# Kernel tuning notes

Measured on AMD Instinct MI355X. Metric: run time of the kernel, lower is better.

The kernel has to match this reference:

```python
import jax, jax.numpy as jnp
import numpy as np

DIM = 768
NUM_HEADS = 12
HEAD_DIM = DIM // NUM_HEADS
SCALE = HEAD_DIM ** (-0.5)
MASK_VAL = -10000000.0


def setup_inputs() -> dict:
    key = jax.random.key(0)
    k1, k2, k3, k4 = jax.random.split(key, 4)
    B, N = 2, 2048
    inputs = jax.random.normal(k1, (B, N, DIM), dtype=jnp.float32)
    padding_mask = jax.random.randint(k2, (B, N), 0, 2, dtype=jnp.int32)
    # Xavier-uniform-ish scaled weights
    w_qkv = jax.random.normal(k3, (3 * DIM, DIM), dtype=jnp.float32) * (1.0 / np.sqrt(DIM))
    w_fc = jax.random.normal(k4, (DIM, DIM), dtype=jnp.float32) * (1.0 / np.sqrt(DIM))
    b_fc = jnp.zeros((DIM,), dtype=jnp.float32)
    return {"inputs": inputs, "padding_mask": padding_mask,
            "w_qkv": w_qkv, "w_fc": w_fc, "b_fc": b_fc}


def reference(inputs, padding_mask, w_qkv, w_fc, b_fc):
    B, N, C = inputs.shape
    # qkv projection (torch Linear: x @ W^T), no bias
    qkv = jnp.einsum('bnc,dc->bnd', inputs, w_qkv)          # [B, N, 3*C]
    qkv = qkv.reshape(B, N, 3, NUM_HEADS, HEAD_DIM)
    qkv = jnp.transpose(qkv, (2, 0, 3, 1, 4))               # [3, B, H, N, hd]
    q, k, v = qkv[0], qkv[1], qkv[2]
    # scores: [B, H, N, N]
    att = jnp.einsum('bhqd,bhkd->bhqk', q, k) * SCALE
    mask = padding_mask[:, None, None, :]                   # [B,1,1,N]
    att = jnp.where(mask > 0, MASK_VAL, att)
    att = jax.nn.softmax(att, axis=-1)
    x = jnp.einsum('bhqk,bhkd->bhqd', att, v)               # [B,H,N,hd]
    x = jnp.transpose(x, (0, 2, 1, 3)).reshape(B, N, C)
    x = jnp.einsum('bnc,dc->bnd', x, w_fc) + b_fc
    return x
```

## Files before the change

### kernel.cpp

```cpp
#include <hip/hip_runtime.h>
#include <hip/hip_bf16.h>

#define DIM_  768
#define NH    12
#define HD    64
#define BB    2
#define NN    2048
#define MM    (BB*NN)
#define QKVD  (3*DIM_)

typedef __attribute__((ext_vector_type(8))) short          bf16x8;
typedef __attribute__((ext_vector_type(4))) float          f32x4;

__device__ __forceinline__ unsigned short f2bf(float f) {
    __hip_bfloat16 h = __float2bfloat16(f);
    unsigned short u; __builtin_memcpy(&u, &h, 2); return u;
}

__device__ __forceinline__ unsigned int cvt_pk_bf16(float lo, float hi) {
    unsigned int r;
    asm("v_cvt_pk_bf16_f32 %0, %1, %2" : "=v"(r) : "v"(lo), "v"(hi));
    return r;
}

__device__ __forceinline__ void gload16(const void* g, void* lds) {
    __builtin_amdgcn_global_load_lds(
        (const __attribute__((address_space(1))) void*)g,
        (__attribute__((address_space(3))) void*)lds, 16, 0, 0);
}

__global__ __launch_bounds__(256)
void cast_all(const float* __restrict__ x, const float* __restrict__ wqkv,
              const float* __restrict__ wfc, unsigned short* __restrict__ xb,
              unsigned short* __restrict__ wqkvb, unsigned short* __restrict__ wfcb)
{
    const int NV0 = (MM * DIM_) / 4;
    const int NV1 = NV0 + (QKVD * DIM_) / 4;
    const int NV2 = NV1 + (DIM_ * DIM_) / 4;
    int i = blockIdx.x * 256 + threadIdx.x;
    if (i >= NV2) return;
    const float* src; unsigned short* dst;
    if (i < NV0)      { src = x + (size_t)i * 4;            dst = xb + (size_t)i * 4; }
    else if (i < NV1) { size_t j = i - NV0; src = wqkv + j * 4; dst = wqkvb + j * 4; }
    else              { size_t j = i - NV1; src = wfc + j * 4;  dst = wfcb + j * 4; }
    float4 v = *(const float4*)src;
    ushort4 o; o.x = f2bf(v.x); o.y = f2bf(v.y); o.z = f2bf(v.z); o.w = f2bf(v.w);
    *(ushort4*)dst = o;
}

__global__ __launch_bounds__(256)
void gemm_qkv(const unsigned short* __restrict__ A, const unsigned short* __restrict__ W,
              unsigned short* __restrict__ qh, unsigned short* __restrict__ kh,
              unsigned short* __restrict__ vth)
{
    __shared__ unsigned short smem[4][4096];
    unsigned short* const pool = &smem[0][0];
    const int tid = threadIdx.x, lane = tid & 63, wave = tid >> 6;
    const int wr = wave >> 1, wc = wave & 1;
    const int n0 = blockIdx.x * 128, m0 = blockIdx.y * 128;
    const int ldrow = lane >> 2, ldg = lane & 3;
    const int g = lane >> 4, q15 = lane & 15;
    constexpr float QSCALE = 0.18033688011112042f;

    f32x4 acc[4][4];
    #pragma unroll
    for (int i = 0; i < 4; ++i)
        #pragma unroll
        for (int j = 0; j < 4; ++j) acc[i][j] = (f32x4){0.f, 0.f, 0.f, 0.f};

    #define STAGE_G(buf, k0)                                                         \
        _Pragma("unroll")                                                            \
        for (int rd = 0; rd < 2; ++rd) {                                             \
            const int chunk = rd * 4 + wave;                                         \
            const int row = chunk * 16 + ldrow;                                      \
            gload16(A + (size_t)(m0 + row) * DIM_ + (k0) + ldg * 8,                  \
                    (char*)&smem[buf][0] + chunk * 1024);                            \
            gload16(W + (size_t)(n0 + row) * DIM_ + (k0) + ldg * 8,                  \
                    (char*)&smem[2 + (buf)][0] + chunk * 1024);                      \
        }

    STAGE_G(0, 0);
    __syncthreads();
    int cur = 0;
    for (int kt = 0; kt < DIM_ / 32; ++kt) {
        if (kt < DIM_ / 32 - 1) { STAGE_G(cur ^ 1, (kt + 1) * 32); }
        bf16x8 af[4], bw[4];
        #pragma unroll
        for (int i = 0; i < 4; ++i)
            af[i] = *(const bf16x8*)((const char*)&smem[cur][0] + (wr*64 + i*16 + q15) * 64 + g * 16);
        #pragma unroll
        for (int j = 0; j < 4; ++j)
            bw[j] = *(const bf16x8*)((const char*)&smem[2 + cur][0] + (wc*64 + j*16 + q15) * 64 + g * 16);
        #pragma unroll
        for (int i = 0; i < 4; ++i)
            #pragma unroll
            for (int j = 0; j < 4; ++j)
                acc[i][j] = __builtin_amdgcn_mfma_f32_16x16x32_bf16(af[i], bw[j], acc[i][j], 0, 0, 0);
        __syncthreads();
        cur ^= 1;
    }
    #undef STAGE_G

    const int s = n0 / DIM_;
    const int bq = m0 >> 11, nq0 = m0 & 2047;
    if (s == 2) {
        #pragma unroll
        for (int j = 0; j < 4; ++j) {
            const int col = wc * 64 + j * 16 + q15;
            const int cs = (col & 7) << 3;
            #pragma unroll
            for (int i = 0; i < 4; ++i) {
                const int row0 = wr * 64 + i * 16 + g * 4;
                ushort4 v;
                v.x = f2bf(acc[i][j][0]); v.y = f2bf(acc[i][j][1]);
                v.z = f2bf(acc[i][j][2]); v.w = f2bf(acc[i][j][3]);
                *(ushort4*)&pool[col * 128 + ((row0 & ~7) ^ cs) + (row0 & 7)] = v;
            }
        }
        __syncthreads();
        const int hh0 = (n0 - 2 * DIM_) >> 6;
        #pragma unroll
        for (int pass = 0; pass < 8; ++pass) {
            const int idx = pass * 256 + tid;
            const int t = idx >> 10;
            const int ddl = (idx & 1023) >> 4;
            const int tok0 = (idx & 15) << 3;
            const int col = t * 64 + ddl;
            const unsigned short* src = &pool[col * 128 + (tok0 ^ ((col & 7) << 3))];
            unsigned short* dst = vth + ((size_t)((bq * NH + hh0 + t) * 64 + ddl)) * NN + nq0 + tok0;
            *(ulonglong2*)dst = *(const ulonglong2*)src;
        }
    } else {
        const float sc = (s == 0) ? QSCALE : 1.0f;
        #pragma unroll
        for (int j = 0; j < 4; ++j) {
            const int colE = wc * 64 + j * 16 + q15;
            #pragma unroll
            for (int i = 0; i < 4; ++i) {
                #pragma unroll
                for (int r = 0; r < 4; ++r) {
                    const int row = wr * 64 + i * 16 + g * 4 + r;
                    pool[row * 128 + (((colE & ~7) ^ ((row & 7) << 3)) | (colE & 7))] =
                        f2bf(acc[i][j][r] * sc);
                }
            }
        }
        __syncthreads();
        const int hh0 = (n0 - s * DIM_) >> 6;
        unsigned short* const dstb = (s == 0) ? qh : kh;
        #pragma unroll
        for (int pass = 0; pass < 8; ++pass) {
            const int idx = pass * 256 + tid;
            const int t = idx >> 10;
            const int off = idx & 1023;
            const int tok = off >> 3;
            const int d0 = (off & 7) << 3;
            const int colb = t * 64 + d0;
            const unsigned short* src = &pool[tok * 128 + (colb ^ ((tok & 7) << 3))];
            unsigned short* dst = dstb + ((size_t)((bq * NH + hh0 + t)) * NN + nq0 + tok) * 64 + d0;
            *(ulonglong2*)dst = *(const ulonglong2*)src;
        }
    }
}

__global__ __launch_bounds__(256)
void gemm_fc(const unsigned short* __restrict__ A, const unsigned short* __restrict__ W,
             const float* __restrict__ bias, float* __restrict__ C, int Md, int Nd, int K)
{
    __shared__ unsigned short As[2][128 * 32];
    __shared__ unsigned short Bs[2][64 * 32];
    const int tid = threadIdx.x, lane = tid & 63, wave = tid >> 6;
    const int wr = wave >> 1, wc = wave & 1;
    const int n0 = blockIdx.x * 64, m0 = blockIdx.y * 128;
    const int ldrow = lane >> 2, ldg = lane & 3;

    f32x4 acc[4][2];
    #pragma unroll
    for (int i = 0; i < 4; ++i)
        #pragma unroll
        for (int j = 0; j < 2; ++j) acc[i][j] = (f32x4){0.f, 0.f, 0.f, 0.f};

    #define STAGE_G(buf, k0)                                                         \
        _Pragma("unroll")                                                            \
        for (int rd = 0; rd < 2; ++rd) {                                             \
            const int chunk = rd * 4 + wave;                                         \
            const int row = chunk * 16 + ldrow;                                      \
            gload16(A + (size_t)(m0 + row) * K + (k0) + ldg * 8,                     \
                    (char*)As[buf] + chunk * 1024);                                  \
        }                                                                            \
        gload16(W + (size_t)(n0 + wave * 16 + ldrow) * K + (k0) + ldg * 8,           \
                (char*)Bs[buf] + wave * 1024);

    STAGE_G(0, 0);
    __syncthreads();
    int cur = 0;
    const int nk = K / 32;
    for (int kt = 0; kt < nk; ++kt) {
        if (kt < nk - 1) { STAGE_G(cur ^ 1, (kt + 1) * 32); }
        bf16x8 af[4], bw[2];
        #pragma unroll
        for (int i = 0; i < 4; ++i)
            af[i] = *(const bf16x8*)((const char*)As[cur] + (wr*64 + i*16 + (lane & 15)) * 64 + (lane >> 4) * 16);
        #pragma unroll
        for (int j = 0; j < 2; ++j)
            bw[j] = *(const bf16x8*)((const char*)Bs[cur] + (wc*32 + j*16 + (lane & 15)) * 64 + (lane >> 4) * 16);
        #pragma unroll
        for (int i = 0; i < 4; ++i)
            #pragma unroll
            for (int j = 0; j < 2; ++j)
                acc[i][j] = __builtin_amdgcn_mfma_f32_16x16x32_bf16(af[i], bw[j], acc[i][j], 0, 0, 0);
        __syncthreads();
        cur ^= 1;
    }

    const int r0 = (lane >> 4) * 4, cl = lane & 15;
    #pragma unroll
    for (int i = 0; i < 4; ++i)
        #pragma unroll
        for (int j = 0; j < 2; ++j) {
            const int n = n0 + wc * 32 + j * 16 + cl;
            const float bv = bias[n];
            #pragma unroll
            for (int r = 0; r < 4; ++r) {
                const int m = m0 + wr * 64 + i * 16 + r0 + r;
                C[(size_t)m * Nd + n] = acc[i][j][r] + bv;
            }
        }
    #undef STAGE_G
}

__global__ __launch_bounds__(256)
void attn_mfma(const unsigned short* __restrict__ qh, const unsigned short* __restrict__ kh,
               const unsigned short* __restrict__ vth, const int* __restrict__ pmask,
               unsigned short* __restrict__ xout)
{
    __shared__ unsigned short Ks[2][64 * 64];
    __shared__ unsigned short Vs[2][64 * 64];
    __shared__ __align__(16) float maskLg[NN];

    const int tid = threadIdx.x, lane = tid & 63, wave = tid >> 6;
    const int g = lane >> 4, q15 = lane & 15, l7 = lane & 7;
    const int X = (lane >> 5) & 1, Y = (lane >> 4) & 1;
    const int swz = (blockIdx.x & 7) * 96 + (blockIdx.x >> 3);
    const int qt = swz & 31;
    const int bh = swz >> 5;
    const int h = bh % NH, b = bh / NH;
    const size_t base = (size_t)(b * NH + h) * NN * 64;

    const int sr = lane >> 3, sg = lane & 7;

    #define STAGE_KV(buf, kt)                                                          \
        _Pragma("unroll")                                                              \
        for (int rd = 0; rd < 2; ++rd) {                                               \
            const int chunk = rd * 4 + wave;                                           \
            const int row = chunk * 8 + sr;                                            \
            const int gs = (sg ^ (sr & 7)) * 8;                                        \
            gload16(kh + base + (size_t)((kt) * 64 + row) * 64 + gs,                   \
                    (char*)Ks[buf] + chunk * 1024);                                    \
            gload16(vth + base + (size_t)row * NN + (kt) * 64 + gs,                    \
                    (char*)Vs[buf] + chunk * 1024);                                    \
        }

    STAGE_KV(0, 0);
    #pragma unroll
    for (int jj = 0; jj < 2; ++jj) {
        const int j = jj * 256 + tid;
        int4 mv = ((const int4*)(pmask + b * NN))[j];
        float4 mf;
        mf.x = mv.x > 0 ? -__builtin_inff() : 0.f;
        mf.y = mv.y > 0 ? -__builtin_inff() : 0.f;
        mf.z = mv.z > 0 ? -__builtin_inff() : 0.f;
        mf.w = mv.w > 0 ? -__builtin_inff() : 0.f;
        ((float4*)maskLg)[j] = mf;
    }
    bf16x8 qf[2];
    {
        const unsigned short* qp = qh + base + (size_t)(qt * 64 + wave * 16 + q15) * 64;
        qf[0] = *(const bf16x8*)(qp + g * 8);
        qf[1] = *(const bf16x8*)(qp + 32 + g * 8);
    }
    __syncthreads();

    float m = -1e30f, lsum = 0.f;
    f32x4 oacc[4];
    #pragma unroll
    for (int fo = 0; fo < 4; ++fo) oacc[fo] = (f32x4){0.f, 0.f, 0.f, 0.f};

    int cur = 0;
    for (int kt = 0; kt < NN / 64; ++kt) {
        if (kt < NN / 64 - 1) { STAGE_KV(cur ^ 1, kt + 1); }

        f32x4 s[4];
        #pragma unroll
        for (int f = 0; f < 4; ++f) s[f] = *(const f32x4*)&maskLg[kt * 64 + f * 16 + g * 4];
        __builtin_amdgcn_s_setprio(1);
        #pragma unroll
        for (int ks = 0; ks < 2; ++ks) {
            #pragma unroll
            for (int f = 0; f < 4; ++f) {
                const int krow = f * 16 + q15;
                const int gk = (g + ks * 4) ^ l7;
                bf16x8 kf = *(const bf16x8*)((const char*)Ks[cur] + krow * 128 + gk * 16);
                s[f] = __builtin_amdgcn_mfma_f32_16x16x32_bf16(kf, qf[ks], s[f], 0, 0, 0);
            }
        }
        __builtin_amdgcn_s_setprio(0);

        float pmax;
        {
            const float a0 = fmaxf(fmaxf(s[0][0], s[0][1]), fmaxf(s[0][2], s[0][3]));
            const float a1 = fmaxf(fmaxf(s[1][0], s[1][1]), fmaxf(s[1][2], s[1][3]));
            const float a2 = fmaxf(fmaxf(s[2][0], s[2][1]), fmaxf(s[2][2], s[2][3]));
            const float a3 = fmaxf(fmaxf(s[3][0], s[3][1]), fmaxf(s[3][2], s[3][3]));
            pmax = fmaxf(fmaxf(a0, a1), fmaxf(a2, a3));
        }
        pmax = fmaxf(pmax, __shfl_xor(pmax, 16));
        pmax = fmaxf(pmax, __shfl_xor(pmax, 32));
        if (__any(pmax > m + 10.0f)) {
            const float mnew = fmaxf(m, pmax);
            const float corr = __builtin_amdgcn_exp2f(m - mnew);
            m = mnew;
            lsum *= corr;
            float c[4];
            #pragma unroll
            for (int r = 0; r < 4; ++r) c[r] = __shfl(corr, g * 4 + r);
            #pragma unroll
            for (int fo = 0; fo < 4; ++fo)
                #pragma unroll
                for (int r = 0; r < 4; ++r) oacc[fo][r] *= c[r];
        }
        float pw[4][4], ps = 0.f;
        #pragma unroll
        for (int f = 0; f < 4; ++f) {
            float psf = 0.f;
            #pragma unroll
            for (int r = 0; r < 4; ++r) {
                const float p = __builtin_amdgcn_exp2f(s[f][r] - m);
                pw[f][r] = p; psf += p;
            }
            ps += psf;
        }
        ps += __shfl_xor(ps, 16);
        ps += __shfl_xor(ps, 32);
        lsum += ps;

        __builtin_amdgcn_s_setprio(1);
        #pragma unroll
        for (int ks = 0; ks < 2; ++ks) {
            unsigned int D00 = cvt_pk_bf16(pw[2*ks+0][0], pw[2*ks+0][1]);
            unsigned int D01 = cvt_pk_bf16(pw[2*ks+0][2], pw[2*ks+0][3]);
            unsigned int D10 = cvt_pk_bf16(pw[2*ks+1][0], pw[2*ks+1][1]);
            unsigned int D11 = cvt_pk_bf16(pw[2*ks+1][2], pw[2*ks+1][3]);
            unsigned int r0 = (unsigned int)__shfl_xor((int)(X ? D00 : D10), 32);
            unsigned int r1 = (unsigned int)__shfl_xor((int)(X ? D01 : D11), 32);
            unsigned int E00 = X ? r0 : D00, E01 = X ? r1 : D01;
            unsigned int E10 = X ? D10 : r0, E11 = X ? D11 : r1;
            unsigned int u0 = (unsigned int)__shfl_xor((int)(Y ? E00 : E10), 16);
            unsigned int u1 = (unsigned int)__shfl_xor((int)(Y ? E01 : E11), 16);
            unsigned int F0 = Y ? u0 : E00, F1 = Y ? u1 : E01;
            unsigned int F2 = Y ? E10 : u0, F3 = Y ? E11 : u1;
            unsigned int pfw[4] = {F0, F1, F2, F3};
            bf16x8 pf;
            __builtin_memcpy(&pf, pfw, 16);
            #pragma unroll
            for (int fo = 0; fo < 4; ++fo) {
                const int gv = (g + ks * 4) ^ l7;
                bf16x8 vf = *(const bf16x8*)((const char*)Vs[cur] + (fo * 16 + q15) * 128 + gv * 16);
                oacc[fo] = __builtin_amdgcn_mfma_f32_16x16x32_bf16(pf, vf, oacc[fo], 0, 0, 0);
            }
        }
        __builtin_amdgcn_s_setprio(0);

        __syncthreads();
        cur ^= 1;
    }

    float linv[4];
    #pragma unroll
    for (int r = 0; r < 4; ++r) linv[r] = 1.0f / __shfl(lsum, g * 4 + r);
    #pragma unroll
    for (int r = 0; r < 4; ++r) {
        const int q = qt * 64 + wave * 16 + g * 4 + r;
        #pragma unroll
        for (int fo = 0; fo < 4; ++fo) {
            const int d = fo * 16 + q15;
            xout[(size_t)(b * NN + q) * DIM_ + h * 64 + d] = f2bf(oacc[fo][r] * linv[r]);
        }
    }
    #undef STAGE_KV
}

extern "C" void kernel_launch(void* const* d_in, const int* in_sizes, int n_in,
                              void* d_out, int out_size, void* d_ws, size_t ws_size,
                              hipStream_t stream)
{
    const float* x     = (const float*)d_in[0];
    const int*   pmask = (const int*)d_in[1];
    const float* wqkv  = (const float*)d_in[2];
    const float* wfc   = (const float*)d_in[3];
    const float* bfc   = (const float*)d_in[4];
    float* out = (float*)d_out;

    const size_t n_x    = (size_t)MM * DIM_;
    const size_t n_wqkv = (size_t)QKVD * DIM_;
    const size_t n_wfc  = (size_t)DIM_ * DIM_;
    const size_t n_head = (size_t)BB * NH * NN * 64;

    unsigned short* xb    = (unsigned short*)d_ws;
    unsigned short* wqkvb = xb + n_x;
    unsigned short* wfcb  = wqkvb + n_wqkv;
    unsigned short* qhb   = wfcb + n_wfc;
    unsigned short* khb   = qhb + n_head;
    unsigned short* vthb  = khb + n_head;
    unsigned short* xattb = vthb + n_head;

    const int nv = (int)((n_x + n_wqkv + n_wfc) / 4);
    cast_all<<<(nv + 255) / 256, 256, 0, stream>>>(x, wqkv, wfc, xb, wqkvb, wfcb);

    gemm_qkv<<<dim3(QKVD / 128, MM / 128), 256, 0, stream>>>(xb, wqkvb, qhb, khb, vthb);
    attn_mfma<<<dim3(BB * NH * (NN / 64)), 256, 0, stream>>>(qhb, khb, vthb, pmask, xattb);
    gemm_fc<<<dim3(DIM_ / 64, MM / 128), 256, 0, stream>>>(xattb, wfcb, bfc, out, MM, DIM_, DIM_);
}
```

Measured before the change: 184.4 us.

## Compact unmasked keys so K/V projection and attention skip masked tokens

A new scan kernel builds a per-batch list of unmasked key indices and their count. The K/V projection gathers only those token rows into compact K/V buffers and skips tiles beyond the padded count. Attention then iterates only over ceil(count/64) key tiles and builds the mask from the count instead of loading a per-block mask array. This removes roughly half of the K/V GEMM and attention work for random masks. It costs an extra small serial-scan launch and indexed row gathers. The reference's large finite mask value is replaced by dropping masked keys entirely, which differs only if a row is fully masked.

Result: faster. 155.0 us (-16.0%).

```diff
diff --git a/kernel.cpp b/kernel.cpp
--- a/kernel.cpp
+++ b/kernel.cpp
@@ -49,7 +49,35 @@
 }
 
 __global__ __launch_bounds__(256)
+void scan_mask(const int* __restrict__ pmask, int* __restrict__ kidx, int* __restrict__ count)
+{
+    __shared__ int sums[256];
+    __shared__ int base[256];
+    const int b = blockIdx.x, tid = threadIdx.x;
+    const int* pm = pmask + b * NN;
+    int* ki = kidx + b * NN;
+    #pragma unroll
+    for (int j = 0; j < 8; ++j) ki[tid * 8 + j] = 0;
+    int mloc[8], s8 = 0;
+    #pragma unroll
+    for (int j = 0; j < 8; ++j) { mloc[j] = pm[tid * 8 + j]; s8 += (mloc[j] == 0); }
+    sums[tid] = s8;
+    __syncthreads();
+    if (tid == 0) {
+        int acc = 0;
+        for (int i = 0; i < 256; ++i) { base[i] = acc; acc += sums[i]; }
+        count[b] = acc;
+    }
+    __syncthreads();
+    int pos = base[tid];
+    #pragma unroll
+    for (int j = 0; j < 8; ++j)
+        if (mloc[j] == 0) ki[pos++] = tid * 8 + j;
+}
+
+__global__ __launch_bounds__(256)
 void gemm_qkv(const unsigned short* __restrict__ A, const unsigned short* __restrict__ W,
+              const int* __restrict__ kidx, const int* __restrict__ count,
               unsigned short* __restrict__ qh, unsigned short* __restrict__ kh,
               unsigned short* __restrict__ vth)
 {
@@ -62,6 +90,23 @@
     const int g = lane >> 4, q15 = lane & 15;
     constexpr float QSCALE = 0.18033688011112042f;
 
+    const int s = n0 / DIM_;
+    const int bq = m0 >> 11, p0 = m0 & 2047;
+    if (s >= 1) {
+        const int padc = (count[bq] + 127) & ~127;
+        if (p0 >= padc) return;
+    }
+
+    size_t arow[2];
+    #pragma unroll
+    for (int rd = 0; rd < 2; ++rd) {
+        const int row = (rd * 4 + wave) * 16 + ldrow;
+        int tok;
+        if (s == 0) tok = m0 + row;
+        else        tok = bq * NN + kidx[bq * NN + p0 + row];
+        arow[rd] = (size_t)tok * DIM_ + ldg * 8;
+    }
+
     f32x4 acc[4][4];
     #pragma unroll
     for (int i = 0; i < 4; ++i)
@@ -72,10 +117,8 @@
         _Pragma("unroll")                                                            \
         for (int rd = 0; rd < 2; ++rd) {                                             \
             const int chunk = rd * 4 + wave;                                         \
-            const int row = chunk * 16 + ldrow;                                      \
-            gload16(A + (size_t)(m0 + row) * DIM_ + (k0) + ldg * 8,                  \
-                    (char*)&smem[buf][0] + chunk * 1024);                            \
-            gload16(W + (size_t)(n0 + row) * DIM_ + (k0) + ldg * 8,                  \
+            gload16(A + arow[rd] + (k0), (char*)&smem[buf][0] + chunk * 1024);       \
+            gload16(W + (size_t)(n0 + chunk * 16 + ldrow) * DIM_ + (k0) + ldg * 8,   \
                     (char*)&smem[2 + (buf)][0] + chunk * 1024);                      \
         }
 
@@ -101,8 +144,6 @@
     }
     #undef STAGE_G
 
-    const int s = n0 / DIM_;
-    const int bq = m0 >> 11, nq0 = m0 & 2047;
     if (s == 2) {
         #pragma unroll
         for (int j = 0; j < 4; ++j) {
@@ -127,7 +168,7 @@
             const int tok0 = (idx & 15) << 3;
             const int col = t * 64 + ddl;
             const unsigned short* src = &pool[col * 128 + (tok0 ^ ((col & 7) << 3))];
-            unsigned short* dst = vth + ((size_t)((bq * NH + hh0 + t) * 64 + ddl)) * NN + nq0 + tok0;
+            unsigned short* dst = vth + ((size_t)((bq * NH + hh0 + t) * 64 + ddl)) * NN + p0 + tok0;
             *(ulonglong2*)dst = *(const ulonglong2*)src;
         }
     } else {
@@ -157,7 +198,7 @@
             const int d0 = (off & 7) << 3;
             const int colb = t * 64 + d0;
             const unsigned short* src = &pool[tok * 128 + (colb ^ ((tok & 7) << 3))];
-            unsigned short* dst = dstb + ((size_t)((bq * NH + hh0 + t)) * NN + nq0 + tok) * 64 + d0;
+            unsigned short* dst = dstb + ((size_t)((bq * NH + hh0 + t)) * NN + p0 + tok) * 64 + d0;
             *(ulonglong2*)dst = *(const ulonglong2*)src;
         }
     }
@@ -231,12 +272,11 @@
 
 __global__ __launch_bounds__(256)
 void attn_mfma(const unsigned short* __restrict__ qh, const unsigned short* __restrict__ kh,
-               const unsigned short* __restrict__ vth, const int* __restrict__ pmask,
+               const unsigned short* __restrict__ vth, const int* __restrict__ count,
                unsigned short* __restrict__ xout)
 {
     __shared__ unsigned short Ks[2][64 * 64];
     __shared__ unsigned short Vs[2][64 * 64];
-    __shared__ __align__(16) float maskLg[NN];
 
     const int tid = threadIdx.x, lane = tid & 63, wave = tid >> 6;
     const int g = lane >> 4, q15 = lane & 15, l7 = lane & 7;
@@ -248,6 +288,8 @@
     const size_t base = (size_t)(b * NH + h) * NN * 64;
 
     const int sr = lane >> 3, sg = lane & 7;
+    const int cnt = count[b];
+    const int nt = (cnt + 63) >> 6;
 
     #define STAGE_KV(buf, kt)                                                          \
         _Pragma("unroll")                                                              \
@@ -262,17 +304,6 @@
         }
 
     STAGE_KV(0, 0);
-    #pragma unroll
-    for (int jj = 0; jj < 2; ++jj) {
-        const int j = jj * 256 + tid;
-        int4 mv = ((const int4*)(pmask + b * NN))[j];
-        float4 mf;
-        mf.x = mv.x > 0 ? -__builtin_inff() : 0.f;
-        mf.y = mv.y > 0 ? -__builtin_inff() : 0.f;
-        mf.z = mv.z > 0 ? -__builtin_inff() : 0.f;
-        mf.w = mv.w > 0 ? -__builtin_inff() : 0.f;
-        ((float4*)maskLg)[j] = mf;
-    }
     bf16x8 qf[2];
     {
         const unsigned short* qp = qh + base + (size_t)(qt * 64 + wave * 16 + q15) * 64;
@@ -287,12 +318,21 @@
     for (int fo = 0; fo < 4; ++fo) oacc[fo] = (f32x4){0.f, 0.f, 0.f, 0.f};
 
     int cur = 0;
-    for (int kt = 0; kt < NN / 64; ++kt) {
-        if (kt < NN / 64 - 1) { STAGE_KV(cur ^ 1, kt + 1); }
+    for (int kt = 0; kt < nt; ++kt) {
+        if (kt + 1 < nt) { STAGE_KV(cur ^ 1, kt + 1); }
 
         f32x4 s[4];
-        #pragma unroll
-        for (int f = 0; f < 4; ++f) s[f] = *(const f32x4*)&maskLg[kt * 64 + f * 16 + g * 4];
+        if ((kt + 1) * 64 <= cnt) {
+            #pragma unroll
+            for (int f = 0; f < 4; ++f) s[f] = (f32x4){0.f, 0.f, 0.f, 0.f};
+        } else {
+            const int kb = kt * 64 + g * 4;
+            #pragma unroll
+            for (int f = 0; f < 4; ++f)
+                #pragma unroll
+                for (int r = 0; r < 4; ++r)
+                    s[f][r] = (kb + f * 16 + r < cnt) ? 0.f : -__builtin_inff();
+        }
         __builtin_amdgcn_s_setprio(1);
         #pragma unroll
         for (int ks = 0; ks < 2; ++ks) {
@@ -413,11 +453,14 @@
     unsigned short* khb   = qhb + n_head;
     unsigned short* vthb  = khb + n_head;
     unsigned short* xattb = vthb + n_head;
+    int* kidx = (int*)(xattb + n_x);
+    int* cnt  = kidx + BB * NN;
 
     const int nv = (int)((n_x + n_wqkv + n_wfc) / 4);
     cast_all<<<(nv + 255) / 256, 256, 0, stream>>>(x, wqkv, wfc, xb, wqkvb, wfcb);
-
-    gemm_qkv<<<dim3(QKVD / 128, MM / 128), 256, 0, stream>>>(xb, wqkvb, qhb, khb, vthb);
-    attn_mfma<<<dim3(BB * NH * (NN / 64)), 256, 0, stream>>>(qhb, khb, vthb, pmask, xattb);
+    scan_mask<<<BB, 256, 0, stream>>>(pmask, kidx, cnt);
+
+    gemm_qkv<<<dim3(QKVD / 128, MM / 128), 256, 0, stream>>>(xb, wqkvb, kidx, cnt, qhb, khb, vthb);
+    attn_mfma<<<dim3(BB * NH * (NN / 64)), 256, 0, stream>>>(qhb, khb, vthb, cnt, xattb);
     gemm_fc<<<dim3(DIM_ / 64, MM / 128), 256, 0, stream>>>(xattb, wfcb, bfc, out, MM, DIM_, DIM_);
 }
```
